# Optimization experiments

Hardware: AMD Instinct MI355X
Metric: run time of the kernel (lower is better)

The kernel has to match this reference:

```python
import jax, jax.numpy as jnp
import numpy as np

B, N, DF = 8, 4096, 768
K1, K2, DS = 8, 2, 128
KVQ, H, ITERS = 128, 1, 3
DH = KVQ // H
EPS_SA = 1e-8
SCALE = DH ** -0.5


def layer_norm(x, g, b, eps=1e-5):
    m = jnp.mean(x, axis=-1, keepdims=True)
    v = jnp.var(x, axis=-1, keepdims=True)
    return (x - m) / jnp.sqrt(v + eps) * g + b


def gru_cell(x, h, Wih, Whh, bih, bhh):
    gi = x @ Wih.T + bih
    gh = h @ Whh.T + bhh
    ir, iz, inn = jnp.split(gi, 3, axis=-1)
    hr, hz, hn = jnp.split(gh, 3, axis=-1)
    r = jax.nn.sigmoid(ir + hr)
    z = jax.nn.sigmoid(iz + hz)
    n = jnp.tanh(inn + r * hn)
    return (1.0 - z) * n + z * h


def setup_inputs() -> dict:
    key = jax.random.key(0)
    ks = jax.random.split(key, 24)
    s = 0.02
    f32 = jnp.float32
    return {
        'tokens': jax.random.normal(ks[0], (B, N, DF), f32),
        'parent_slots': jax.random.normal(ks[1], (B, K1, DS), f32),
        'parent_masks': jax.random.uniform(ks[2], (B, K1, N), f32),
        'eps_noise': jax.random.normal(ks[3], (B, K1, K2, DS), f32),
        'ln_in_g': jnp.ones((DF,), f32), 'ln_in_b': jnp.zeros((DF,), f32),
        'ln_s_g': jnp.ones((DS,), f32), 'ln_s_b': jnp.zeros((DS,), f32),
        'Wq': jax.random.normal(ks[4], (KVQ, DS), f32) * s,
        'Wk': jax.random.normal(ks[5], (KVQ, DF), f32) * s,
        'Wv': jax.random.normal(ks[6], (KVQ, DF), f32) * s,
        'gru_Wih': jax.random.normal(ks[7], (3 * DS, KVQ), f32) * s,
        'gru_Whh': jax.random.normal(ks[8], (3 * DS, DS), f32) * s,
        'gru_bih': jnp.zeros((3 * DS,), f32),
        'gru_bhh': jnp.zeros((3 * DS,), f32),
        'mlp_ln_g': jnp.ones((DS,), f32), 'mlp_ln_b': jnp.zeros((DS,), f32),
        'mlp_W1': jax.random.normal(ks[9], (4 * DS, DS), f32) * s,
        'mlp_b1': jnp.zeros((4 * DS,), f32),
        'mlp_W2': jax.random.normal(ks[10], (DS, 4 * DS), f32) * s,
        'mlp_b2': jnp.zeros((DS,), f32),
    }


def reference(tokens, parent_slots, parent_masks, eps_noise,
              ln_in_g, ln_in_b, ln_s_g, ln_s_b, Wq, Wk, Wv,
              gru_Wih, gru_Whh, gru_bih, gru_bhh,
              mlp_ln_g, mlp_ln_b, mlp_W1, mlp_b1, mlp_W2, mlp_b2):
    BK = B * K1
    # parent-mask gating (all parents vectorized, folded into batch)
    denom = jnp.mean(parent_masks, axis=-1, keepdims=True)          # [B,K1,1]
    safe = (denom > 1e-6).astype(tokens.dtype)
    w_scaled = safe * (parent_masks / (denom + 1e-6)) + (1.0 - safe)  # [B,K1,N]
    tg = (tokens[:, None, :, :] * w_scaled[..., None]).reshape(BK, N, DF)
    slots = (parent_slots[:, :, None, :] + 0.01 * eps_noise).reshape(BK, K2, DS)

    inp = layer_norm(tg, ln_in_g, ln_in_b)
    k = (inp @ Wk.T).reshape(BK, N, H, DH)
    v = (inp @ Wv.T).reshape(BK, N, H, DH)

    attn_bw = None
    for _ in range(ITERS):
        slots_prev = slots
        sn = layer_norm(slots, ln_s_g, ln_s_b)
        q = (sn @ Wq.T).reshape(BK, K2, H, DH)
        dots = jnp.einsum('bihd,bjhd->bihj', q, k) * SCALE          # [BK,K2,H,N]
        attn = jax.nn.softmax(dots, axis=1) + EPS_SA                # softmax over slots
        attn_bw = attn
        attn_w = attn / jnp.sum(attn, axis=-1, keepdims=True)
        updates = jnp.einsum('bjhd,bihj->bihd', v, attn_w).reshape(BK * K2, KVQ)
        slots = gru_cell(updates, slots_prev.reshape(BK * K2, DS),
                         gru_Wih, gru_Whh, gru_bih, gru_bhh).reshape(BK, K2, DS)
        h = layer_norm(slots, mlp_ln_g, mlp_ln_b)
        slots = jax.nn.gelu(h @ mlp_W1.T + mlp_b1, approximate=False) @ mlp_W2.T + mlp_b2

    attn_out = jnp.mean(attn_bw, axis=2)                            # [BK,K2,N]
    child_objects = slots.reshape(B, K1 * K2, DS)
    child_gating = (attn_out.reshape(B, K1, K2, N) * parent_masks[:, :, None, :]).reshape(B, K1 * K2, N)
    return child_objects, child_gating
```

## Files before the change

### kernel.cpp

```cpp
#include <hip/hip_runtime.h>
#include <math.h>

#define SCALE_ 0.08838834764831843f

typedef __attribute__((ext_vector_type(8))) short bf16x8;
typedef __attribute__((ext_vector_type(4))) float f32x4;

static const size_t OFF_VAR   = 0;
static const size_t OFF_DENOM = 32768;
static const size_t OFF_GSUM  = 32832;
static const size_t OFF_BIAS  = 33088;
static const size_t OFF_QKB   = 33344;
static const size_t OFF_SSUM  = 33472;
static const size_t OFF_SLOTS = 33600;
static const size_t OFF_Q     = 49984;
static const size_t OFF_WQBF  = 66368;
static const size_t OFF_WIHBF = 74560;
static const size_t OFF_WHHBF = 99136;
static const size_t OFF_W1BF  = 123712;
static const size_t OFF_WM2BF = 156480;
static const size_t OFF_WKVBF = 189248;
static const size_t OFF_UPART = 287552;
static const size_t OFF_KB    = 1336128;
static const size_t OFF_VT    = 3433280;

__device__ __forceinline__ float wred64(float v) {
#pragma unroll
  for (int off = 32; off > 0; off >>= 1) v += __shfl_xor(v, off, 64);
  return v;
}

__device__ __forceinline__ unsigned short f2bf(float f) {
  unsigned u = __float_as_uint(f);
  unsigned r = (u + 0x7fffu + ((u >> 16) & 1u)) >> 16;
  return (unsigned short)r;
}

__device__ __forceinline__ unsigned pack2(float a, float b) {
  return (unsigned)f2bf(a) | ((unsigned)f2bf(b) << 16);
}

__global__ __launch_bounds__(256) void prep_all_k(
    const float* __restrict__ Wk, const float* __restrict__ Wv,
    const float* __restrict__ g, const float* __restrict__ bb,
    const float* __restrict__ Wq, const float* __restrict__ Wih,
    const float* __restrict__ Whh, const float* __restrict__ W1,
    const float* __restrict__ W2, const float* __restrict__ pm,
    unsigned short* __restrict__ wkv, float* __restrict__ gsum,
    float* __restrict__ biasArr,
    unsigned short* __restrict__ Wqbf, unsigned short* __restrict__ Wihbf,
    unsigned short* __restrict__ Whhbf, unsigned short* __restrict__ W1bf,
    unsigned short* __restrict__ Wm2bf, float* __restrict__ denomArr)
{
  __shared__ float red4[4];
  int bi = blockIdx.x, t = threadIdx.x;
  if (bi < 64) {
    int j = bi*4 + (t >> 6), lane = t & 63;
    const float* w = (j < 128) ? (Wk + (size_t)j*768) : (Wv + (size_t)(j-128)*768);
    float gs = 0.f, bs = 0.f;
#pragma unroll
    for (int s = 0; s < 12; ++s) {
      int dd = lane + s*64;
      float wv = w[dd], gv = g[dd];
      gs += gv*wv; bs += bb[dd]*wv;
      wkv[(size_t)j*768 + dd] = f2bf(wv*gv);
    }
    gs = wred64(gs); bs = wred64(bs);
    if (lane == 0) { gsum[j] = gs; biasArr[j] = bs; }
  } else if (bi < 128) {
    int idx = (bi-64)*256 + t;  Wqbf[idx]  = f2bf(Wq[idx]);
  } else if (bi < 320) {
    int idx = (bi-128)*256 + t; Wihbf[idx] = f2bf(Wih[idx]);
  } else if (bi < 512) {
    int idx = (bi-320)*256 + t; Whhbf[idx] = f2bf(Whh[idx]);
  } else if (bi < 768) {
    int idx = (bi-512)*256 + t; W1bf[idx]  = f2bf(W1[idx]);
  } else if (bi < 1024) {
    int idx = (bi-768)*256 + t; Wm2bf[idx] = f2bf(W2[idx]);
  } else {
    int bk = bi - 1024;
    float s = 0.f;
#pragma unroll
    for (int k = 0; k < 16; ++k) s += pm[bk*4096 + t + k*256];
    s = wred64(s);
    if ((t & 63) == 0) red4[t >> 6] = s;
    __syncthreads();
    if (t == 0) denomArr[bk] = (red4[0]+red4[1]+red4[2]+red4[3])*(1.f/4096.f);
  }
}

__global__ __launch_bounds__(256) void gemm_kv_k(
    const float* __restrict__ tokens, const unsigned short* __restrict__ wkv,
    const float* __restrict__ gsum, unsigned short* __restrict__ Kb,
    unsigned short* __restrict__ VT, float* __restrict__ varArr)
{
  int bi = blockIdx.x;
  int r0 = bi*64;
  int t = threadIdx.x;
  int w = t >> 6, ln = t & 63;
  int lm = ln & 15, lq = ln >> 4;
  int rowbase = r0 + (w >> 1)*32;
  int colbase = (w & 1)*128;

  const float* a0p = tokens + (size_t)(rowbase + lm)*768 + lq*8;
  const float* a1p = tokens + (size_t)(rowbase + 16 + lm)*768 + lq*8;
  const unsigned short* bp = wkv + (size_t)(colbase + lm)*768 + lq*8;

  f32x4 acc[2][8];
#pragma unroll
  for (int a = 0; a < 2; ++a)
#pragma unroll
    for (int c = 0; c < 8; ++c) acc[a][c] = f32x4{0.f, 0.f, 0.f, 0.f};
  float s1a = 0.f, s2a = 0.f, s1b = 0.f, s2b = 0.f;

  float4 cA0a = *(const float4*)(a0p);
  float4 cA0b = *(const float4*)(a0p + 4);
  float4 cA1a = *(const float4*)(a1p);
  float4 cA1b = *(const float4*)(a1p + 4);
  bf16x8 Bf[2][8];
#pragma unroll
  for (int nt = 0; nt < 8; ++nt)
    Bf[0][nt] = *(const bf16x8*)(bp + (size_t)(nt*16)*768);

#pragma unroll 2
  for (int k = 0; k < 24; ++k) {
    const int kb = k & 1;
    float4 nA0a, nA0b, nA1a, nA1b;
    if (k < 23) {
      const float* a0n = a0p + (k+1)*32;
      const float* a1n = a1p + (k+1)*32;
      nA0a = *(const float4*)(a0n);
      nA0b = *(const float4*)(a0n + 4);
      nA1a = *(const float4*)(a1n);
      nA1b = *(const float4*)(a1n + 4);
#pragma unroll
      for (int nt = 0; nt < 8; ++nt)
        Bf[kb ^ 1][nt] = *(const bf16x8*)(bp + (size_t)(nt*16)*768 + (k+1)*32);
    }
    s1a += cA0a.x + cA0a.y + cA0a.z + cA0a.w + cA0b.x + cA0b.y + cA0b.z + cA0b.w;
    s2a += cA0a.x*cA0a.x + cA0a.y*cA0a.y + cA0a.z*cA0a.z + cA0a.w*cA0a.w
         + cA0b.x*cA0b.x + cA0b.y*cA0b.y + cA0b.z*cA0b.z + cA0b.w*cA0b.w;
    s1b += cA1a.x + cA1a.y + cA1a.z + cA1a.w + cA1b.x + cA1b.y + cA1b.z + cA1b.w;
    s2b += cA1a.x*cA1a.x + cA1a.y*cA1a.y + cA1a.z*cA1a.z + cA1a.w*cA1a.w
         + cA1b.x*cA1b.x + cA1b.y*cA1b.y + cA1b.z*cA1b.z + cA1b.w*cA1b.w;
    bf16x8 af0, af1;
    { uint4 tmp = make_uint4(pack2(cA0a.x, cA0a.y), pack2(cA0a.z, cA0a.w),
                             pack2(cA0b.x, cA0b.y), pack2(cA0b.z, cA0b.w));
      af0 = *(bf16x8*)&tmp; }
    { uint4 tmp = make_uint4(pack2(cA1a.x, cA1a.y), pack2(cA1a.z, cA1a.w),
                             pack2(cA1b.x, cA1b.y), pack2(cA1b.z, cA1b.w));
      af1 = *(bf16x8*)&tmp; }
#pragma unroll
    for (int nt = 0; nt < 8; ++nt) {
      acc[0][nt] = __builtin_amdgcn_mfma_f32_16x16x32_bf16(af0, Bf[kb][nt], acc[0][nt], 0, 0, 0);
      acc[1][nt] = __builtin_amdgcn_mfma_f32_16x16x32_bf16(af1, Bf[kb][nt], acc[1][nt], 0, 0, 0);
    }
    cA0a = nA0a; cA0b = nA0b; cA1a = nA1a; cA1b = nA1b;
  }

  s1a += __shfl_xor(s1a, 16, 64); s1a += __shfl_xor(s1a, 32, 64);
  s2a += __shfl_xor(s2a, 16, 64); s2a += __shfl_xor(s2a, 32, 64);
  s1b += __shfl_xor(s1b, 16, 64); s1b += __shfl_xor(s1b, 32, 64);
  s2b += __shfl_xor(s2b, 16, 64); s2b += __shfl_xor(s2b, 32, 64);
  float mean0 = s1a*(1.f/768.f), var0 = s2a*(1.f/768.f) - mean0*mean0;
  float mean1 = s1b*(1.f/768.f), var1 = s2b*(1.f/768.f) - mean1*mean1;
  if ((w & 1) == 0 && lq == 0) {
    varArr[rowbase + lm] = var0;
    varArr[rowbase + 16 + lm] = var1;
  }
  float m0R[4], m1R[4];
#pragma unroll
  for (int reg = 0; reg < 4; ++reg) {
    m0R[reg] = __shfl(mean0, lq*4 + reg, 64);
    m1R[reg] = __shfl(mean1, lq*4 + reg, 64);
  }

  if ((w & 1) == 0) {
#pragma unroll
    for (int nt = 0; nt < 8; ++nt) {
      int col = nt*16 + lm;
      float gs = gsum[col];
#pragma unroll
      for (int T = 0; T < 2; ++T) {
#pragma unroll
        for (int reg = 0; reg < 4; ++reg) {
          int tok = rowbase + T*16 + lq*4 + reg;
          float mv = T ? m1R[reg] : m0R[reg];
          Kb[(size_t)tok*128 + col] = f2bf(acc[T][nt][reg] - mv*gs);
        }
      }
    }
  } else {
#pragma unroll
    for (int nt = 0; nt < 8; ++nt) {
      int d = nt*16 + lm;
      float gs = gsum[128 + d];
#pragma unroll
      for (int T = 0; T < 2; ++T) {
        int tok0 = rowbase + T*16 + lq*4;
        int b = tok0 >> 12;
        int n = tok0 & 4095;
        float m0 = T ? m1R[0] : m0R[0];
        float m1 = T ? m1R[1] : m0R[1];
        float m2 = T ? m1R[2] : m0R[2];
        float m3 = T ? m1R[3] : m0R[3];
        ushort4 v;
        v.x = f2bf(acc[T][nt][0] - m0*gs);
        v.y = f2bf(acc[T][nt][1] - m1*gs);
        v.z = f2bf(acc[T][nt][2] - m2*gs);
        v.w = f2bf(acc[T][nt][3] - m3*gs);
        *(ushort4*)&VT[((size_t)(b*128 + d))*4096 + n] = v;
      }
    }
  }
}

__global__ __launch_bounds__(256, 1) void slots_init_q_k(
    const float* __restrict__ ps, const float* __restrict__ eps,
    const float* __restrict__ g_s, const float* __restrict__ b_s,
    const unsigned short* __restrict__ Wqbf, const float* __restrict__ biasArr,
    float* __restrict__ slots, float* __restrict__ qg, float* __restrict__ qkb,
    float* __restrict__ Ssum)
{
  __shared__ unsigned short Fsn[2048];
  __shared__ float qkbL[16];
  int R0 = blockIdx.x*16;
  int t = threadIdx.x;
  int w = t >> 6, ln = t & 63, lm = ln & 15, lq = ln >> 4;
  if (t < 16) qkbL[t] = 0.f;
  {
    int r = t >> 4, dseg = t & 15, ds8 = dseg*8;
    int row = R0 + r, bk = row >> 1;
    float xv[8]; float s1 = 0.f, s2 = 0.f;
#pragma unroll
    for (int j = 0; j < 8; ++j) {
      int d = ds8 + j;
      float x = ps[bk*128 + d] + 0.01f*eps[row*128 + d];
      slots[row*128 + d] = x;
      xv[j] = x; s1 += x; s2 += x*x;
    }
#pragma unroll
    for (int m = 8; m >= 1; m >>= 1) {
      s1 += __shfl_xor(s1, m, 16);
      s2 += __shfl_xor(s2, m, 16);
    }
    float mean = s1*(1.f/128.f);
    float var = s2*(1.f/128.f) - mean*mean;
    float rstd = rsqrtf(var + 1e-5f);
    float sv[8];
#pragma unroll
    for (int j = 0; j < 8; ++j) {
      int d = ds8 + j;
      sv[j] = (xv[j] - mean)*rstd*g_s[d] + b_s[d];
    }
    int fa = ((dseg >> 2)*64 + (dseg & 3)*16 + r)*8;
    *(uint4*)&Fsn[fa] = make_uint4(pack2(sv[0],sv[1]), pack2(sv[2],sv[3]),
                                   pack2(sv[4],sv[5]), pack2(sv[6],sv[7]));
  }
  __syncthreads();
  {
    bf16x8 af[4];
#pragma unroll
    for (int kc = 0; kc < 4; ++kc)
      af[kc] = *(const bf16x8*)(&Fsn[(kc*64 + ln)*8]);
    float pr[4] = {0.f, 0.f, 0.f, 0.f};
#pragma unroll
    for (int i = 0; i < 2; ++i) {
      int n0 = w*32 + i*16;
      f32x4 acc = f32x4{0.f,0.f,0.f,0.f};
#pragma unroll
      for (int kc = 0; kc < 4; ++kc) {
        bf16x8 bw = *(const bf16x8*)(&Wqbf[(size_t)(n0+lm)*128 + kc*32 + lq*8]);
        acc = __builtin_amdgcn_mfma_f32_16x16x32_bf16(af[kc], bw, acc, 0,0,0);
      }
      int n = n0 + lm;
      float bk_ = biasArr[n];
#pragma unroll
      for (int reg = 0; reg < 4; ++reg) {
        int row = lq*4 + reg;
        qg[(size_t)(R0 + row)*128 + n] = acc[reg];
        pr[reg] += acc[reg]*bk_;
      }
    }
#pragma unroll
    for (int reg = 0; reg < 4; ++reg) {
#pragma unroll
      for (int m = 8; m >= 1; m >>= 1) pr[reg] += __shfl_xor(pr[reg], m, 16);
    }
    if (lm == 0) {
#pragma unroll
      for (int reg = 0; reg < 4; ++reg)
        atomicAdd(&qkbL[lq*4 + reg], pr[reg]);
    }
  }
  __syncthreads();
  if (t < 16) { qkb[R0 + t] = qkbL[t]; Ssum[R0 + t] = 0.f; }
}

__global__ __launch_bounds__(128) void attn_fused_k(
    const unsigned short* __restrict__ Kb, const unsigned short* __restrict__ VT,
    const float* __restrict__ qg, const float* __restrict__ qkb,
    const float* __restrict__ varArr, const float* __restrict__ denomArr,
    const float* __restrict__ pm,
    float* __restrict__ Upart, float* __restrict__ Ssum,
    float* __restrict__ outG, int last)
{
  __shared__ unsigned short Pl[2][16*68];
  int bi = blockIdx.x;
  int b = bi >> 5, nch = bi & 31;
  int t = threadIdx.x;
  int wv = t >> 6, ln = t & 63;
  int lm = ln & 15, lq = ln >> 4;
  int ntok0 = nch*128 + wv*64;
  unsigned short* pl = &Pl[wv][0];

  bf16x8 qf[4];
#pragma unroll
  for (int kc = 0; kc < 4; ++kc) {
    const float* qp = qg + (size_t)(b*16 + lm)*128 + kc*32 + lq*8;
    float4 q0 = *(const float4*)qp;
    float4 q1 = *(const float4*)(qp + 4);
    uint4 tmp = make_uint4(pack2(q0.x,q0.y), pack2(q0.z,q0.w),
                           pack2(q1.x,q1.y), pack2(q1.z,q1.w));
    qf[kc] = *(bf16x8*)&tmp;
  }
  float qkbv[4];
#pragma unroll
  for (int reg = 0; reg < 4; ++reg) qkbv[reg] = qkb[b*16 + lq*4 + reg];
  float den0 = denomArr[b*8 + lq*2];
  float den1 = denomArr[b*8 + lq*2 + 1];
  bool g0 = den0 > 1e-6f, g1 = den1 > 1e-6f;
  float inv0 = 1.f/(den0 + 1e-6f), inv1 = 1.f/(den1 + 1e-6f);

  f32x4 Uacc[8];
#pragma unroll
  for (int dt = 0; dt < 8; ++dt) Uacc[dt] = f32x4{0.f,0.f,0.f,0.f};
  float sAcc[4] = {0.f, 0.f, 0.f, 0.f};

#pragma unroll
  for (int half = 0; half < 2; ++half) {
    int tk0 = ntok0 + half*32;
#pragma unroll
    for (int ti = 0; ti < 2; ++ti) {
      int n0 = tk0 + ti*16;
      int n = n0 + lm;
      f32x4 dacc = f32x4{0.f,0.f,0.f,0.f};
      const unsigned short* kp = Kb + ((size_t)(b*4096 + n))*128 + lq*8;
#pragma unroll
      for (int kc = 0; kc < 4; ++kc) {
        bf16x8 kf = *(const bf16x8*)(kp + kc*32);
        dacc = __builtin_amdgcn_mfma_f32_16x16x32_bf16(qf[kc], kf, dacc, 0,0,0);
      }
      float vv = varArr[b*4096 + n];
      float pm0 = pm[((size_t)(b*8 + lq*2))*4096 + n];
      float pm1 = pm[((size_t)(b*8 + lq*2 + 1))*4096 + n];
      float c0 = g0 ? pm0*inv0 : 1.f;
      float c1 = g1 ? pm1*inv1 : 1.f;
      float al0 = c0*rsqrtf(c0*c0*vv + 1e-5f);
      float al1 = c1*rsqrtf(c1*c1*vv + 1e-5f);
      float dd0 = SCALE_*(al0*dacc[0] + qkbv[0]);
      float dd1 = SCALE_*(al0*dacc[1] + qkbv[1]);
      float mx0 = fmaxf(dd0, dd1);
      float e0 = expf(dd0 - mx0), e1 = expf(dd1 - mx0);
      float is0 = 1.f/(e0 + e1);
      float o0 = e0*is0 + 1e-8f, o1 = e1*is0 + 1e-8f;
      float dd2 = SCALE_*(al1*dacc[2] + qkbv[2]);
      float dd3 = SCALE_*(al1*dacc[3] + qkbv[3]);
      float mx1 = fmaxf(dd2, dd3);
      float e2 = expf(dd2 - mx1), e3 = expf(dd3 - mx1);
      float is1 = 1.f/(e2 + e3);
      float o2 = e2*is1 + 1e-8f, o3 = e3*is1 + 1e-8f;
      sAcc[0] += o0; sAcc[1] += o1; sAcc[2] += o2; sAcc[3] += o3;
      if (last) {
        size_t ob = ((size_t)(b*16 + lq*4))*4096 + n;
        outG[ob]          = o0*pm0;
        outG[ob + 4096]   = o1*pm0;
        outG[ob + 8192]   = o2*pm1;
        outG[ob + 12288]  = o3*pm1;
      }
      int pc = half*32 + ti*16 + lm;
      pl[(lq*4 + 0)*68 + pc] = f2bf(o0*al0);
      pl[(lq*4 + 1)*68 + pc] = f2bf(o1*al0);
      pl[(lq*4 + 2)*68 + pc] = f2bf(o2*al1);
      pl[(lq*4 + 3)*68 + pc] = f2bf(o3*al1);
    }
    bf16x8 pf = *(const bf16x8*)&pl[lm*68 + half*32 + lq*8];
    const unsigned short* vp = VT + ((size_t)(b*128 + lm))*4096 + tk0 + lq*8;
#pragma unroll
    for (int dt = 0; dt < 8; ++dt) {
      bf16x8 vf = *(const bf16x8*)(vp + (size_t)(dt*16)*4096);
      Uacc[dt] = __builtin_amdgcn_mfma_f32_16x16x32_bf16(pf, vf, Uacc[dt], 0,0,0);
    }
  }

#pragma unroll
  for (int reg = 0; reg < 4; ++reg) {
    float r = sAcc[reg];
    r += __shfl_xor(r, 1, 64); r += __shfl_xor(r, 2, 64);
    r += __shfl_xor(r, 4, 64); r += __shfl_xor(r, 8, 64);
    if (lm == 0) atomicAdd(&Ssum[b*16 + lq*4 + reg], r);
  }
  float* up = Upart + ((size_t)(b*64 + nch*2 + wv))*2048;
#pragma unroll
  for (int dt = 0; dt < 8; ++dt)
#pragma unroll
    for (int reg = 0; reg < 4; ++reg)
      up[(lq*4 + reg)*128 + dt*16 + lm] = Uacc[dt][reg];
}

__global__ __launch_bounds__(256, 1) void gru_mlp_q_k(
    const float* __restrict__ Upart, const float* __restrict__ Ssum,
    const float* __restrict__ biasArr,
    const unsigned short* __restrict__ Wihbf, const unsigned short* __restrict__ Whhbf,
    const float* __restrict__ bih, const float* __restrict__ bhh,
    const float* __restrict__ mlp_g, const float* __restrict__ mlp_b,
    const unsigned short* __restrict__ W1bf, const float* __restrict__ b1,
    const unsigned short* __restrict__ Wm2bf, const float* __restrict__ b2,
    const float* __restrict__ ln_s_g, const float* __restrict__ ln_s_b,
    const unsigned short* __restrict__ Wqbf,
    float* __restrict__ slots, float* __restrict__ qg, float* __restrict__ qkb,
    float* __restrict__ SsumW, float* __restrict__ outObj, int last)
{
  __shared__ unsigned short FXx[2048], FXh[2048], Fhn[2048], Fsn[2048];
  __shared__ unsigned short Ft1[8192];
  __shared__ float G_rz[16*256];
  __shared__ float G_in[16*128];
  __shared__ float G_hn[16*128];
  __shared__ float hs_[16*128];
  __shared__ float os_[16*128];
  __shared__ float qkbL[16];

  int R0 = blockIdx.x*16;
  int t = threadIdx.x;
  int w = t >> 6, ln = t & 63;
  int lm = ln & 15, lq = ln >> 4;

  {
    int r = t >> 4, dseg = t & 15, ds8 = dseg*8;
    int R = R0 + r;
    float ua[8];
#pragma unroll
    for (int j = 0; j < 8; ++j) ua[j] = 0.f;
    const float* up = Upart + (size_t)blockIdx.x*131072 + r*128 + ds8;
#pragma unroll 8
    for (int ch = 0; ch < 64; ++ch) {
      float4 u0 = *(const float4*)(up + (size_t)ch*2048);
      float4 u1 = *(const float4*)(up + (size_t)ch*2048 + 4);
      ua[0]+=u0.x; ua[1]+=u0.y; ua[2]+=u0.z; ua[3]+=u0.w;
      ua[4]+=u1.x; ua[5]+=u1.y; ua[6]+=u1.z; ua[7]+=u1.w;
    }
    float Sv = 1.f/Ssum[R];
    float4 bv0 = *(const float4*)(biasArr + 128 + ds8);
    float4 bv1 = *(const float4*)(biasArr + 132 + ds8);
    float xv[8];
    xv[0]=ua[0]*Sv+bv0.x; xv[1]=ua[1]*Sv+bv0.y; xv[2]=ua[2]*Sv+bv0.z; xv[3]=ua[3]*Sv+bv0.w;
    xv[4]=ua[4]*Sv+bv1.x; xv[5]=ua[5]*Sv+bv1.y; xv[6]=ua[6]*Sv+bv1.z; xv[7]=ua[7]*Sv+bv1.w;
    float4 h0 = *(const float4*)(slots + (size_t)R*128 + ds8);
    float4 h1 = *(const float4*)(slots + (size_t)R*128 + ds8 + 4);
    *(float4*)(hs_ + r*128 + ds8) = h0;
    *(float4*)(hs_ + r*128 + ds8 + 4) = h1;
    int fa = ((dseg >> 2)*64 + (dseg & 3)*16 + r)*8;
    *(uint4*)&FXx[fa] = make_uint4(pack2(xv[0],xv[1]), pack2(xv[2],xv[3]),
                                   pack2(xv[4],xv[5]), pack2(xv[6],xv[7]));
    *(uint4*)&FXh[fa] = make_uint4(pack2(h0.x,h0.y), pack2(h0.z,h0.w),
                                   pack2(h1.x,h1.y), pack2(h1.z,h1.w));
    if (t < 16) qkbL[t] = 0.f;
  }
  __syncthreads();

  {
    bf16x8 ax[4], ah[4];
#pragma unroll
    for (int kc = 0; kc < 4; ++kc) {
      ax[kc] = *(const bf16x8*)(&FXx[(kc*64 + ln)*8]);
      ah[kc] = *(const bf16x8*)(&FXh[(kc*64 + ln)*8]);
    }
    if (w < 2) {
#pragma unroll
      for (int i = 0; i < 8; ++i) {
        int n0 = (w*8 + i)*16;
        f32x4 acc = f32x4{0.f,0.f,0.f,0.f};
#pragma unroll
        for (int kc = 0; kc < 4; ++kc) {
          bf16x8 bi_ = *(const bf16x8*)(&Wihbf[(size_t)(n0+lm)*128 + kc*32 + lq*8]);
          acc = __builtin_amdgcn_mfma_f32_16x16x32_bf16(ax[kc], bi_, acc, 0,0,0);
        }
#pragma unroll
        for (int kc = 0; kc < 4; ++kc) {
          bf16x8 bh_ = *(const bf16x8*)(&Whhbf[(size_t)(n0+lm)*128 + kc*32 + lq*8]);
          acc = __builtin_amdgcn_mfma_f32_16x16x32_bf16(ah[kc], bh_, acc, 0,0,0);
        }
#pragma unroll
        for (int reg = 0; reg < 4; ++reg)
          G_rz[(lq*4+reg)*256 + n0 + lm] = acc[reg];
      }
    } else if (w == 2) {
#pragma unroll
      for (int i = 0; i < 8; ++i) {
        int n0 = 256 + i*16;
        f32x4 acc = f32x4{0.f,0.f,0.f,0.f};
#pragma unroll
        for (int kc = 0; kc < 4; ++kc) {
          bf16x8 bi_ = *(const bf16x8*)(&Wihbf[(size_t)(n0+lm)*128 + kc*32 + lq*8]);
          acc = __builtin_amdgcn_mfma_f32_16x16x32_bf16(ax[kc], bi_, acc, 0,0,0);
        }
#pragma unroll
        for (int reg = 0; reg < 4; ++reg)
          G_in[(lq*4+reg)*128 + i*16 + lm] = acc[reg];
      }
    } else {
#pragma unroll
      for (int i = 0; i < 8; ++i) {
        int n0 = 256 + i*16;
        f32x4 acc = f32x4{0.f,0.f,0.f,0.f};
#pragma unroll
        for (int kc = 0; kc < 4; ++kc) {
          bf16x8 bh_ = *(const bf16x8*)(&Whhbf[(size_t)(n0+lm)*128 + kc*32 + lq*8]);
          acc = __builtin_amdgcn_mfma_f32_16x16x32_bf16(ah[kc], bh_, acc, 0,0,0);
        }
#pragma unroll
        for (int reg = 0; reg < 4; ++reg)
          G_hn[(lq*4+reg)*128 + i*16 + lm] = acc[reg];
      }
    }
  }
  __syncthreads();

  {
    int r = t >> 4, dseg = t & 15, ds8 = dseg*8;
    float hp[8];
    float s1 = 0.f, s2 = 0.f;
#pragma unroll
    for (int j = 0; j < 8; ++j) {
      int d = ds8 + j;
      float rg = G_rz[r*256 + d] + bih[d] + bhh[d];
      float zg = G_rz[r*256 + 128 + d] + bih[128+d] + bhh[128+d];
      float ing = G_in[r*128 + d] + bih[256+d];
      float hng = G_hn[r*128 + d] + bhh[256+d];
      float rv = 1.f/(1.f + expf(-rg));
      float zv = 1.f/(1.f + expf(-zg));
      float nv = tanhf(ing + rv*hng);
      float h0 = hs_[r*128 + d];
      float h = (1.f - zv)*nv + zv*h0;
      hp[j] = h;
      s1 += h; s2 += h*h;
    }
#pragma unroll
    for (int m = 8; m >= 1; m >>= 1) {
      s1 += __shfl_xor(s1, m, 16);
      s2 += __shfl_xor(s2, m, 16);
    }
    float mean = s1*(1.f/128.f);
    float var = s2*(1.f/128.f) - mean*mean;
    float rstd = rsqrtf(var + 1e-5f);
    float hv[8];
#pragma unroll
    for (int j = 0; j < 8; ++j) {
      int d = ds8 + j;
      hv[j] = (hp[j] - mean)*rstd*mlp_g[d] + mlp_b[d];
    }
    int fa = ((dseg >> 2)*64 + (dseg & 3)*16 + r)*8;
    *(uint4*)&Fhn[fa] = make_uint4(pack2(hv[0],hv[1]), pack2(hv[2],hv[3]),
                                   pack2(hv[4],hv[5]), pack2(hv[6],hv[7]));
  }
  __syncthreads();

  {
    bf16x8 af[4];
#pragma unroll
    for (int kc = 0; kc < 4; ++kc)
      af[kc] = *(const bf16x8*)(&Fhn[(kc*64 + ln)*8]);
#pragma unroll
    for (int i = 0; i < 8; ++i) {
      int n0 = (w*8 + i)*16;
      f32x4 acc = f32x4{0.f,0.f,0.f,0.f};
#pragma unroll
      for (int kc = 0; kc < 4; ++kc) {
        bf16x8 bw = *(const bf16x8*)(&W1bf[(size_t)(n0+lm)*128 + kc*32 + lq*8]);
        acc = __builtin_amdgcn_mfma_f32_16x16x32_bf16(af[kc], bw, acc, 0,0,0);
      }
      int kdim = n0 + lm;
      float bb = b1[kdim];
      int kc2 = kdim >> 5;
      int sub = (kdim >> 3) & 3;
      int jj = kdim & 7;
#pragma unroll
      for (int reg = 0; reg < 4; ++reg) {
        float v = acc[reg] + bb;
        float gel = 0.5f*v*(1.f + erff(v*0.70710678118654752f));
        Ft1[(kc2*64 + sub*16 + lq*4 + reg)*8 + jj] = f2bf(gel);
      }
    }
  }
  __syncthreads();

  {
#pragma unroll
    for (int i = 0; i < 2; ++i) {
      int n0 = w*32 + i*16;
      f32x4 acc = f32x4{0.f,0.f,0.f,0.f};
#pragma unroll
      for (int kc = 0; kc < 16; ++kc) {
        bf16x8 af = *(const bf16x8*)(&Ft1[(kc*64 + ln)*8]);
        bf16x8 bw = *(const bf16x8*)(&Wm2bf[(size_t)(n0+lm)*512 + kc*32 + lq*8]);
        acc = __builtin_amdgcn_mfma_f32_16x16x32_bf16(af, bw, acc, 0,0,0);
      }
      int n = n0 + lm;
      float bb = b2[n];
#pragma unroll
      for (int reg = 0; reg < 4; ++reg) {
        int row = lq*4 + reg;
        float o = acc[reg] + bb;
        slots[(size_t)(R0 + row)*128 + n] = o;
        os_[row*128 + n] = o;
        if (last) outObj[(size_t)(R0 + row)*128 + n] = o;
      }
    }
  }

  if (last) return;

  __syncthreads();
  {
    int r = t >> 4, dseg = t & 15, ds8 = dseg*8;
    float ov[8];
    float s1 = 0.f, s2 = 0.f;
#pragma unroll
    for (int j = 0; j < 8; ++j) {
      float o = os_[r*128 + ds8 + j];
      ov[j] = o; s1 += o; s2 += o*o;
    }
#pragma unroll
    for (int m = 8; m >= 1; m >>= 1) {
      s1 += __shfl_xor(s1, m, 16);
      s2 += __shfl_xor(s2, m, 16);
    }
    float mean = s1*(1.f/128.f);
    float var = s2*(1.f/128.f) - mean*mean;
    float rstd = rsqrtf(var + 1e-5f);
    float sv[8];
#pragma unroll
    for (int j = 0; j < 8; ++j) {
      int d = ds8 + j;
      sv[j] = (ov[j] - mean)*rstd*ln_s_g[d] + ln_s_b[d];
    }
    int fa = ((dseg >> 2)*64 + (dseg & 3)*16 + r)*8;
    *(uint4*)&Fsn[fa] = make_uint4(pack2(sv[0],sv[1]), pack2(sv[2],sv[3]),
                                   pack2(sv[4],sv[5]), pack2(sv[6],sv[7]));
  }
  __syncthreads();

  {
    bf16x8 af[4];
#pragma unroll
    for (int kc = 0; kc < 4; ++kc)
      af[kc] = *(const bf16x8*)(&Fsn[(kc*64 + ln)*8]);
    float pr[4] = {0.f, 0.f, 0.f, 0.f};
#pragma unroll
    for (int i = 0; i < 2; ++i) {
      int n0 = w*32 + i*16;
      f32x4 acc = f32x4{0.f,0.f,0.f,0.f};
#pragma unroll
      for (int kc = 0; kc < 4; ++kc) {
        bf16x8 bw = *(const bf16x8*)(&Wqbf[(size_t)(n0+lm)*128 + kc*32 + lq*8]);
        acc = __builtin_amdgcn_mfma_f32_16x16x32_bf16(af[kc], bw, acc, 0,0,0);
      }
      int n = n0 + lm;
      float bk_ = biasArr[n];
#pragma unroll
      for (int reg = 0; reg < 4; ++reg) {
        int row = lq*4 + reg;
        qg[(size_t)(R0 + row)*128 + n] = acc[reg];
        pr[reg] += acc[reg]*bk_;
      }
    }
#pragma unroll
    for (int reg = 0; reg < 4; ++reg) {
#pragma unroll
      for (int m = 8; m >= 1; m >>= 1) pr[reg] += __shfl_xor(pr[reg], m, 16);
    }
    if (lm == 0) {
#pragma unroll
      for (int reg = 0; reg < 4; ++reg)
        atomicAdd(&qkbL[lq*4 + reg], pr[reg]);
    }
  }
  __syncthreads();
  if (t < 16) {
    qkb[R0 + t] = qkbL[t];
    SsumW[R0 + t] = 0.f;
  }
}

extern "C" void kernel_launch(void* const* d_in, const int* in_sizes, int n_in,
                              void* d_out, int out_size, void* d_ws, size_t ws_size,
                              hipStream_t stream) {
  const float* tokens = (const float*)d_in[0];
  const float* pslots = (const float*)d_in[1];
  const float* pmasks = (const float*)d_in[2];
  const float* eps    = (const float*)d_in[3];
  const float* ln_in_g= (const float*)d_in[4];
  const float* ln_in_b= (const float*)d_in[5];
  const float* ln_s_g = (const float*)d_in[6];
  const float* ln_s_b = (const float*)d_in[7];
  const float* Wq     = (const float*)d_in[8];
  const float* Wk     = (const float*)d_in[9];
  const float* Wv     = (const float*)d_in[10];
  const float* Wih    = (const float*)d_in[11];
  const float* Whh    = (const float*)d_in[12];
  const float* bih    = (const float*)d_in[13];
  const float* bhh    = (const float*)d_in[14];
  const float* mlp_g  = (const float*)d_in[15];
  const float* mlp_b  = (const float*)d_in[16];
  const float* W1     = (const float*)d_in[17];
  const float* b1     = (const float*)d_in[18];
  const float* W2     = (const float*)d_in[19];
  const float* b2     = (const float*)d_in[20];
  float* ws  = (float*)d_ws;
  float* out = (float*)d_out;
  unsigned short* wkvbf = (unsigned short*)(ws + OFF_WKVBF);
  unsigned short* wqbf  = (unsigned short*)(ws + OFF_WQBF);
  unsigned short* wihbf = (unsigned short*)(ws + OFF_WIHBF);
  unsigned short* whhbf = (unsigned short*)(ws + OFF_WHHBF);
  unsigned short* w1bf  = (unsigned short*)(ws + OFF_W1BF);
  unsigned short* wm2bf = (unsigned short*)(ws + OFF_WM2BF);
  unsigned short* kb    = (unsigned short*)(ws + OFF_KB);
  unsigned short* vt    = (unsigned short*)(ws + OFF_VT);

  prep_all_k<<<1088, 256, 0, stream>>>(Wk, Wv, ln_in_g, ln_in_b,
                                       Wq, Wih, Whh, W1, W2, pmasks,
                                       wkvbf, ws + OFF_GSUM, ws + OFF_BIAS,
                                       wqbf, wihbf, whhbf, w1bf, wm2bf,
                                       ws + OFF_DENOM);
  gemm_kv_k<<<512, 256, 0, stream>>>(tokens, wkvbf, ws + OFF_GSUM,
                                     kb, vt, ws + OFF_VAR);
  slots_init_q_k<<<8, 256, 0, stream>>>(pslots, eps, ln_s_g, ln_s_b,
                                        wqbf, ws + OFF_BIAS,
                                        ws + OFF_SLOTS, ws + OFF_Q,
                                        ws + OFF_QKB, ws + OFF_SSUM);
  for (int it = 0; it < 3; ++it) {
    int last = (it == 2);
    attn_fused_k<<<256, 128, 0, stream>>>(kb, vt, ws + OFF_Q, ws + OFF_QKB,
                                          ws + OFF_VAR, ws + OFF_DENOM, pmasks,
                                          ws + OFF_UPART, ws + OFF_SSUM,
                                          out + 16384, last);
    gru_mlp_q_k<<<8, 256, 0, stream>>>(ws + OFF_UPART, ws + OFF_SSUM,
                                       ws + OFF_BIAS, wihbf, whhbf, bih, bhh,
                                       mlp_g, mlp_b, w1bf, b1, wm2bf, b2,
                                       ln_s_g, ln_s_b, wqbf,
                                       ws + OFF_SLOTS, ws + OFF_Q, ws + OFF_QKB,
                                       ws + OFF_SSUM, out, last);
  }
}
```

Before: 376.5 us.

## Stage KV GEMM through swizzled LDS and fold mean correction into weights

The K/V projection GEMM now stages token and weight tiles in LDS, using global_load_lds for the weights and an XOR swizzle to avoid bank conflicts. Before, each wave loaded its operands straight from global memory. The layer-norm mean term is folded into the weights by centering them (w*g minus the row mean), which removes the gsum array and the per-output mean subtraction. The attention kernel also adds its two waves' partial updates in shared memory before writing, which halves the Upart traffic and the number of chunks the GRU kernel reduces. Costs are extra block barriers and LDS pressure, plus bf16 rounding of the centered weights, which may shift numerics slightly.

```diff
diff --git a/kernel.cpp b/kernel.cpp
--- a/kernel.cpp
+++ b/kernel.cpp
@@ -1,4 +1,5 @@
 #include <hip/hip_runtime.h>
+#include <hip/hip_bf16.h>
 #include <math.h>
 
 #define SCALE_ 0.08838834764831843f
@@ -37,7 +38,11 @@
 }
 
 __device__ __forceinline__ unsigned pack2(float a, float b) {
-  return (unsigned)f2bf(a) | ((unsigned)f2bf(b) << 16);
+  float2 f; f.x = a; f.y = b;
+  __hip_bfloat162 h = __float22bfloat162_rn(f);
+  unsigned r;
+  __builtin_memcpy(&r, &h, 4);
+  return r;
 }
 
 __global__ __launch_bounds__(256) void prep_all_k(
@@ -46,8 +51,7 @@
     const float* __restrict__ Wq, const float* __restrict__ Wih,
     const float* __restrict__ Whh, const float* __restrict__ W1,
     const float* __restrict__ W2, const float* __restrict__ pm,
-    unsigned short* __restrict__ wkv, float* __restrict__ gsum,
-    float* __restrict__ biasArr,
+    unsigned short* __restrict__ wkv, float* __restrict__ biasArr,
     unsigned short* __restrict__ Wqbf, unsigned short* __restrict__ Wihbf,
     unsigned short* __restrict__ Whhbf, unsigned short* __restrict__ W1bf,
     unsigned short* __restrict__ Wm2bf, float* __restrict__ denomArr)
@@ -58,15 +62,24 @@
     int j = bi*4 + (t >> 6), lane = t & 63;
     const float* w = (j < 128) ? (Wk + (size_t)j*768) : (Wv + (size_t)(j-128)*768);
     float gs = 0.f, bs = 0.f;
+    float st[12];
+    int key = j & 7;
 #pragma unroll
     for (int s = 0; s < 12; ++s) {
       int dd = lane + s*64;
       float wv = w[dd], gv = g[dd];
-      gs += gv*wv; bs += bb[dd]*wv;
-      wkv[(size_t)j*768 + dd] = f2bf(wv*gv);
+      st[s] = wv*gv;
+      gs += st[s]; bs += bb[dd]*wv;
     }
     gs = wred64(gs); bs = wred64(bs);
-    if (lane == 0) { gsum[j] = gs; biasArr[j] = bs; }
+    float corr = gs*(1.f/768.f);
+#pragma unroll
+    for (int s = 0; s < 12; ++s) {
+      int dd = lane + s*64;
+      int sw = (dd & ~63) | (((((dd >> 3) & 7) ^ key)) << 3) | (dd & 7);
+      wkv[(size_t)j*768 + sw] = f2bf(st[s] - corr);
+    }
+    if (lane == 0) biasArr[j] = bs;
   } else if (bi < 128) {
     int idx = (bi-64)*256 + t;  Wqbf[idx]  = f2bf(Wq[idx]);
   } else if (bi < 320) {
@@ -91,102 +104,92 @@
 
 __global__ __launch_bounds__(256) void gemm_kv_k(
     const float* __restrict__ tokens, const unsigned short* __restrict__ wkv,
-    const float* __restrict__ gsum, unsigned short* __restrict__ Kb,
-    unsigned short* __restrict__ VT, float* __restrict__ varArr)
+    unsigned short* __restrict__ Kb, unsigned short* __restrict__ VT,
+    float* __restrict__ varArr)
 {
-  int bi = blockIdx.x;
-  int r0 = bi*64;
+  __shared__ unsigned short As[64*64];
+  __shared__ unsigned short Bs[256*64];
+  int r0 = blockIdx.x*64;
   int t = threadIdx.x;
-  int w = t >> 6, ln = t & 63;
-  int lm = ln & 15, lq = ln >> 4;
-  int rowbase = r0 + (w >> 1)*32;
-  int colbase = (w & 1)*128;
-
-  const float* a0p = tokens + (size_t)(rowbase + lm)*768 + lq*8;
-  const float* a1p = tokens + (size_t)(rowbase + 16 + lm)*768 + lq*8;
-  const unsigned short* bp = wkv + (size_t)(colbase + lm)*768 + lq*8;
+  int w = t >> 6, lane = t & 63;
+  int lm = lane & 15, lq = lane >> 4;
+  int g16 = t >> 4, seg = t & 15;
+  int m0 = (w >> 1)*32, n0 = (w & 1)*128;
 
   f32x4 acc[2][8];
 #pragma unroll
   for (int a = 0; a < 2; ++a)
 #pragma unroll
     for (int c = 0; c < 8; ++c) acc[a][c] = f32x4{0.f, 0.f, 0.f, 0.f};
-  float s1a = 0.f, s2a = 0.f, s1b = 0.f, s2b = 0.f;
-
-  float4 cA0a = *(const float4*)(a0p);
-  float4 cA0b = *(const float4*)(a0p + 4);
-  float4 cA1a = *(const float4*)(a1p);
-  float4 cA1b = *(const float4*)(a1p + 4);
-  bf16x8 Bf[2][8];
-#pragma unroll
-  for (int nt = 0; nt < 8; ++nt)
-    Bf[0][nt] = *(const bf16x8*)(bp + (size_t)(nt*16)*768);
-
-#pragma unroll 2
-  for (int k = 0; k < 24; ++k) {
-    const int kb = k & 1;
-    float4 nA0a, nA0b, nA1a, nA1b;
-    if (k < 23) {
-      const float* a0n = a0p + (k+1)*32;
-      const float* a1n = a1p + (k+1)*32;
-      nA0a = *(const float4*)(a0n);
-      nA0b = *(const float4*)(a0n + 4);
-      nA1a = *(const float4*)(a1n);
-      nA1b = *(const float4*)(a1n + 4);
-#pragma unroll
-      for (int nt = 0; nt < 8; ++nt)
-        Bf[kb ^ 1][nt] = *(const bf16x8*)(bp + (size_t)(nt*16)*768 + (k+1)*32);
-    }
-    s1a += cA0a.x + cA0a.y + cA0a.z + cA0a.w + cA0b.x + cA0b.y + cA0b.z + cA0b.w;
-    s2a += cA0a.x*cA0a.x + cA0a.y*cA0a.y + cA0a.z*cA0a.z + cA0a.w*cA0a.w
-         + cA0b.x*cA0b.x + cA0b.y*cA0b.y + cA0b.z*cA0b.z + cA0b.w*cA0b.w;
-    s1b += cA1a.x + cA1a.y + cA1a.z + cA1a.w + cA1b.x + cA1b.y + cA1b.z + cA1b.w;
-    s2b += cA1a.x*cA1a.x + cA1a.y*cA1a.y + cA1a.z*cA1a.z + cA1a.w*cA1a.w
-         + cA1b.x*cA1b.x + cA1b.y*cA1b.y + cA1b.z*cA1b.z + cA1b.w*cA1b.w;
-    bf16x8 af0, af1;
-    { uint4 tmp = make_uint4(pack2(cA0a.x, cA0a.y), pack2(cA0a.z, cA0a.w),
-                             pack2(cA0b.x, cA0b.y), pack2(cA0b.z, cA0b.w));
-      af0 = *(bf16x8*)&tmp; }
-    { uint4 tmp = make_uint4(pack2(cA1a.x, cA1a.y), pack2(cA1a.z, cA1a.w),
-                             pack2(cA1b.x, cA1b.y), pack2(cA1b.z, cA1b.w));
-      af1 = *(bf16x8*)&tmp; }
-#pragma unroll
-    for (int nt = 0; nt < 8; ++nt) {
-      acc[0][nt] = __builtin_amdgcn_mfma_f32_16x16x32_bf16(af0, Bf[kb][nt], acc[0][nt], 0, 0, 0);
-      acc[1][nt] = __builtin_amdgcn_mfma_f32_16x16x32_bf16(af1, Bf[kb][nt], acc[1][nt], 0, 0, 0);
-    }
-    cA0a = nA0a; cA0b = nA0b; cA1a = nA1a; cA1b = nA1b;
-  }
-
-  s1a += __shfl_xor(s1a, 16, 64); s1a += __shfl_xor(s1a, 32, 64);
-  s2a += __shfl_xor(s2a, 16, 64); s2a += __shfl_xor(s2a, 32, 64);
-  s1b += __shfl_xor(s1b, 16, 64); s1b += __shfl_xor(s1b, 32, 64);
-  s2b += __shfl_xor(s2b, 16, 64); s2b += __shfl_xor(s2b, 32, 64);
-  float mean0 = s1a*(1.f/768.f), var0 = s2a*(1.f/768.f) - mean0*mean0;
-  float mean1 = s1b*(1.f/768.f), var1 = s2b*(1.f/768.f) - mean1*mean1;
-  if ((w & 1) == 0 && lq == 0) {
-    varArr[rowbase + lm] = var0;
-    varArr[rowbase + 16 + lm] = var1;
-  }
-  float m0R[4], m1R[4];
-#pragma unroll
-  for (int reg = 0; reg < 4; ++reg) {
-    m0R[reg] = __shfl(mean0, lq*4 + reg, 64);
-    m1R[reg] = __shfl(mean1, lq*4 + reg, 64);
-  }
-
+  float s1[4] = {0.f,0.f,0.f,0.f}, s2[4] = {0.f,0.f,0.f,0.f};
+
+  for (int k0 = 0; k0 < 768; k0 += 64) {
+    __syncthreads();
+#pragma unroll
+    for (int s = 0; s < 8; ++s) {
+      int row = w*64 + s*8;
+      __builtin_amdgcn_global_load_lds(
+        (const __attribute__((address_space(1))) void*)
+          (wkv + (size_t)(row + (lane >> 3))*768 + k0 + (lane & 7)*8),
+        (__attribute__((address_space(3))) void*)(&Bs[row*64]), 16, 0, 0);
+    }
+#pragma unroll
+    for (int p = 0; p < 4; ++p) {
+      int row = p*16 + g16;
+      float4 x = *(const float4*)(tokens + (size_t)(r0 + row)*768 + k0 + seg*4);
+      s1[p] += x.x + x.y + x.z + x.w;
+      s2[p] += x.x*x.x + x.y*x.y + x.z*x.z + x.w*x.w;
+      int off = row*64 + (((seg >> 1) ^ (row & 7)) << 3) + (seg & 1)*4;
+      *(uint2*)(&As[off]) = make_uint2(pack2(x.x, x.y), pack2(x.z, x.w));
+    }
+    __syncthreads();
+#pragma unroll
+    for (int kk8 = 0; kk8 < 8; kk8 += 4) {
+      bf16x8 af[2], bfr[8];
+#pragma unroll
+      for (int mt = 0; mt < 2; ++mt) {
+        int row = m0 + mt*16 + lm;
+        af[mt] = *(const bf16x8*)(&As[row*64 + (((kk8 + lq) ^ (row & 7)) << 3)]);
+      }
+#pragma unroll
+      for (int nt = 0; nt < 8; ++nt) {
+        int row = n0 + nt*16 + lm;
+        bfr[nt] = *(const bf16x8*)(&Bs[row*64 + (((kk8 + lq) ^ (row & 7)) << 3)]);
+      }
+#pragma unroll
+      for (int mt = 0; mt < 2; ++mt)
+#pragma unroll
+        for (int nt = 0; nt < 8; ++nt)
+          acc[mt][nt] = __builtin_amdgcn_mfma_f32_16x16x32_bf16(
+              af[mt], bfr[nt], acc[mt][nt], 0, 0, 0);
+    }
+  }
+#pragma unroll
+  for (int p = 0; p < 4; ++p) {
+#pragma unroll
+    for (int m = 8; m >= 1; m >>= 1) {
+      s1[p] += __shfl_xor(s1[p], m, 16);
+      s2[p] += __shfl_xor(s2[p], m, 16);
+    }
+  }
+  if (seg == 0) {
+#pragma unroll
+    for (int p = 0; p < 4; ++p) {
+      int row = p*16 + g16;
+      float m = s1[p]*(1.f/768.f);
+      varArr[r0 + row] = s2[p]*(1.f/768.f) - m*m;
+    }
+  }
   if ((w & 1) == 0) {
 #pragma unroll
     for (int nt = 0; nt < 8; ++nt) {
       int col = nt*16 + lm;
-      float gs = gsum[col];
-#pragma unroll
-      for (int T = 0; T < 2; ++T) {
+#pragma unroll
+      for (int mt = 0; mt < 2; ++mt) {
 #pragma unroll
         for (int reg = 0; reg < 4; ++reg) {
-          int tok = rowbase + T*16 + lq*4 + reg;
-          float mv = T ? m1R[reg] : m0R[reg];
-          Kb[(size_t)tok*128 + col] = f2bf(acc[T][nt][reg] - mv*gs);
+          int tok = r0 + m0 + mt*16 + lq*4 + reg;
+          Kb[(size_t)tok*128 + col] = f2bf(acc[mt][nt][reg]);
         }
       }
     }
@@ -194,22 +197,14 @@
 #pragma unroll
     for (int nt = 0; nt < 8; ++nt) {
       int d = nt*16 + lm;
-      float gs = gsum[128 + d];
-#pragma unroll
-      for (int T = 0; T < 2; ++T) {
-        int tok0 = rowbase + T*16 + lq*4;
+#pragma unroll
+      for (int mt = 0; mt < 2; ++mt) {
+        int tok0 = r0 + m0 + mt*16 + lq*4;
         int b = tok0 >> 12;
         int n = tok0 & 4095;
-        float m0 = T ? m1R[0] : m0R[0];
-        float m1 = T ? m1R[1] : m0R[1];
-        float m2 = T ? m1R[2] : m0R[2];
-        float m3 = T ? m1R[3] : m0R[3];
-        ushort4 v;
-        v.x = f2bf(acc[T][nt][0] - m0*gs);
-        v.y = f2bf(acc[T][nt][1] - m1*gs);
-        v.z = f2bf(acc[T][nt][2] - m2*gs);
-        v.w = f2bf(acc[T][nt][3] - m3*gs);
-        *(ushort4*)&VT[((size_t)(b*128 + d))*4096 + n] = v;
+        uint2 v = make_uint2(pack2(acc[mt][nt][0], acc[mt][nt][1]),
+                             pack2(acc[mt][nt][2], acc[mt][nt][3]));
+        *(uint2*)&VT[((size_t)(b*128 + d))*4096 + n] = v;
       }
     }
   }
@@ -306,6 +301,7 @@
     float* __restrict__ outG, int last)
 {
   __shared__ unsigned short Pl[2][16*68];
+  __shared__ float Upw[2][2048];
   int bi = blockIdx.x;
   int b = bi >> 5, nch = bi & 31;
   int t = threadIdx.x;
@@ -400,12 +396,22 @@
     r += __shfl_xor(r, 4, 64); r += __shfl_xor(r, 8, 64);
     if (lm == 0) atomicAdd(&Ssum[b*16 + lq*4 + reg], r);
   }
-  float* up = Upart + ((size_t)(b*64 + nch*2 + wv))*2048;
+  float* uw = &Upw[wv][0];
 #pragma unroll
   for (int dt = 0; dt < 8; ++dt)
 #pragma unroll
     for (int reg = 0; reg < 4; ++reg)
-      up[(lq*4 + reg)*128 + dt*16 + lm] = Uacc[dt][reg];
+      uw[(lq*4 + reg)*128 + dt*16 + lm] = Uacc[dt][reg];
+  __syncthreads();
+  float* up = Upart + (size_t)(b*32 + nch)*2048;
+#pragma unroll
+  for (int i = 0; i < 4; ++i) {
+    int idx = t*16 + i*4;
+    float4 a = *(const float4*)&Upw[0][idx];
+    float4 c = *(const float4*)&Upw[1][idx];
+    float4 o; o.x = a.x + c.x; o.y = a.y + c.y; o.z = a.z + c.z; o.w = a.w + c.w;
+    *(float4*)&up[idx] = o;
+  }
 }
 
 __global__ __launch_bounds__(256, 1) void gru_mlp_q_k(
@@ -441,9 +447,9 @@
     float ua[8];
 #pragma unroll
     for (int j = 0; j < 8; ++j) ua[j] = 0.f;
-    const float* up = Upart + (size_t)blockIdx.x*131072 + r*128 + ds8;
+    const float* up = Upart + (size_t)blockIdx.x*65536 + r*128 + ds8;
 #pragma unroll 8
-    for (int ch = 0; ch < 64; ++ch) {
+    for (int ch = 0; ch < 32; ++ch) {
       float4 u0 = *(const float4*)(up + (size_t)ch*2048);
       float4 u1 = *(const float4*)(up + (size_t)ch*2048 + 4);
       ua[0]+=u0.x; ua[1]+=u0.y; ua[2]+=u0.z; ua[3]+=u0.w;
@@ -729,11 +735,10 @@
 
   prep_all_k<<<1088, 256, 0, stream>>>(Wk, Wv, ln_in_g, ln_in_b,
                                        Wq, Wih, Whh, W1, W2, pmasks,
-                                       wkvbf, ws + OFF_GSUM, ws + OFF_BIAS,
+                                       wkvbf, ws + OFF_BIAS,
                                        wqbf, wihbf, whhbf, w1bf, wm2bf,
                                        ws + OFF_DENOM);
-  gemm_kv_k<<<512, 256, 0, stream>>>(tokens, wkvbf, ws + OFF_GSUM,
-                                     kb, vt, ws + OFF_VAR);
+  gemm_kv_k<<<512, 256, 0, stream>>>(tokens, wkvbf, kb, vt, ws + OFF_VAR);
   slots_init_q_k<<<8, 256, 0, stream>>>(pslots, eps, ln_s_g, ln_s_b,
                                         wqbf, ws + OFF_BIAS,
                                         ws + OFF_SLOTS, ws + OFF_Q,
```

New measurement: 332.3 us. 1.13x faster.
